# Kernel optimization log

Hardware: AMD Instinct MI355X
Metric: run time of the kernel (lower is better)

## Reference

```python
import jax, jax.numpy as jnp
from jax import lax
import numpy as np

B, T, Z, H, W = 4, 256, 16, 64, 64

def setup_inputs() -> dict:
    key = jax.random.key(0)
    k1, k2, k3, k4, k5 = jax.random.split(key, 5)
    # per-pixel scalar RNN parameters (nn.RNN(1, 1) per pixel)
    return {
        "x": jax.random.normal(k1, (B, T, Z, H, W), dtype=jnp.float32),
        "w_ih": jax.random.normal(k2, (Z, H, W), dtype=jnp.float32),
        "w_hh": jax.random.normal(k3, (Z, H, W), dtype=jnp.float32),
        "b_ih": jax.random.normal(k4, (Z, H, W), dtype=jnp.float32),
        "b_hh": jax.random.normal(k5, (Z, H, W), dtype=jnp.float32),
    }

def reference(x, w_ih, w_hh, b_ih, b_hh):
    # x: (B, T, Z, H, W). Per-pixel scalar tanh-RNN, h0 = 0:
    #   h_t = tanh(w_ih * x_t + b_ih + w_hh * h_{t-1} + b_hh)
    xt = jnp.moveaxis(x, 1, 0)  # (T, B, Z, H, W) for scan over time
    bias = b_ih + b_hh          # fuse biases once

    def step(h, x_t):
        h_new = jnp.tanh(x_t * w_ih + h * w_hh + bias)
        return h_new, h_new

    h0 = jnp.zeros(xt.shape[1:], dtype=x.dtype)  # (B, Z, H, W)
    _, ys = lax.scan(step, h0, xt)               # ys: (T, B, Z, H, W)
    return jnp.moveaxis(ys, 0, 1)                # (B, T, Z, H, W)
```

## Files before the change

kernel.cpp:

```cpp
#include <hip/hip_runtime.h>


#define RNN_B   4
#define RNN_T   256
#define RNN_ZHW 65536
#define RNN_PG4 (RNN_ZHW / 4)
#define PF_D    8

typedef float f32x4 __attribute__((ext_vector_type(4)));

__device__ __forceinline__ float fast_tanh(float x) {
    float e = __builtin_amdgcn_exp2f(x * 2.885390081777927f);
    float r = __builtin_amdgcn_rcpf(e + 1.0f);
    return fmaf(-2.0f, r, 1.0f);
}

__global__ __launch_bounds__(256) void pixel_rnn_kernel(
    const float* __restrict__ x,
    const float* __restrict__ w_ih,
    const float* __restrict__ w_hh,
    const float* __restrict__ b_ih,
    const float* __restrict__ b_hh,
    float* __restrict__ out)
{
    const int g  = blockIdx.x * 256 + threadIdx.x;
    const int b  = g >> 14;
    const int pg = g & (RNN_PG4 - 1);
    const int p  = pg << 2;

    const f32x4 wi = *(const f32x4*)(w_ih + p);
    const f32x4 wh = *(const f32x4*)(w_hh + p);
    const f32x4 bi = *(const f32x4*)(b_ih + p);
    const f32x4 bh = *(const f32x4*)(b_hh + p);
    const f32x4 bias = bi + bh;

    const f32x4* __restrict__ xp = (const f32x4*)x + (size_t)b * (RNN_T * RNN_PG4) + pg;
    f32x4* __restrict__ op       = (f32x4*)out     + (size_t)b * (RNN_T * RNN_PG4) + pg;

    f32x4 h = {0.f, 0.f, 0.f, 0.f};

    f32x4 buf[PF_D];
#pragma unroll
    for (int j = 0; j < PF_D; ++j)
        buf[j] = __builtin_nontemporal_load(xp + (size_t)j * RNN_PG4);

    for (int t = 0; t < RNN_T; t += PF_D) {
#pragma unroll
        for (int j = 0; j < PF_D; ++j) {
            const f32x4 xc = buf[j];
            int tn = t + j + PF_D;
            tn = tn < RNN_T ? tn : RNN_T - 1;
            buf[j] = __builtin_nontemporal_load(xp + (size_t)tn * RNN_PG4);

#pragma unroll
            for (int c = 0; c < 4; ++c)
                h[c] = fast_tanh(fmaf(wi[c], xc[c], fmaf(wh[c], h[c], bias[c])));

            __builtin_nontemporal_store(h, op + (size_t)(t + j) * RNN_PG4);
        }
    }
}

extern "C" void kernel_launch(void* const* d_in, const int* in_sizes, int n_in,
                              void* d_out, int out_size, void* d_ws, size_t ws_size,
                              hipStream_t stream) {
    const float* x    = (const float*)d_in[0];
    const float* w_ih = (const float*)d_in[1];
    const float* w_hh = (const float*)d_in[2];
    const float* b_ih = (const float*)d_in[3];
    const float* b_hh = (const float*)d_in[4];
    float* out        = (float*)d_out;

    pixel_rnn_kernel<<<dim3(RNN_B * RNN_PG4 / 256), dim3(256), 0, stream>>>(
        x, w_ih, w_hh, b_ih, b_hh, out);
}
```

Measured before the change: 434.3 us.

## Switch from float4-per-thread to scalar-per-thread pixels and peel prefetch tail

Each thread now handles one pixel instead of four, which launches four times as many threads (1024 blocks instead of 256) to raise occupancy and memory-level parallelism across the 256 CUs. Loads and stores become scalar 4-byte accesses, which stay coalesced across the wavefront but issue more memory instructions. The clamped prefetch index is replaced by a peeled final iteration, which removes the redundant tail loads.

```diff
diff --git a/kernel.cpp b/kernel.cpp
--- a/kernel.cpp
+++ b/kernel.cpp
@@ -4,10 +4,7 @@
 #define RNN_B   4
 #define RNN_T   256
 #define RNN_ZHW 65536
-#define RNN_PG4 (RNN_ZHW / 4)
 #define PF_D    8
-
-typedef float f32x4 __attribute__((ext_vector_type(4)));
 
 __device__ __forceinline__ float fast_tanh(float x) {
     float e = __builtin_amdgcn_exp2f(x * 2.885390081777927f);
@@ -23,41 +20,39 @@
     const float* __restrict__ b_hh,
     float* __restrict__ out)
 {
-    const int g  = blockIdx.x * 256 + threadIdx.x;
-    const int b  = g >> 14;
-    const int pg = g & (RNN_PG4 - 1);
-    const int p  = pg << 2;
+    const int g = blockIdx.x * 256 + threadIdx.x;
+    const int b = g >> 16;
+    const int p = g & (RNN_ZHW - 1);
 
-    const f32x4 wi = *(const f32x4*)(w_ih + p);
-    const f32x4 wh = *(const f32x4*)(w_hh + p);
-    const f32x4 bi = *(const f32x4*)(b_ih + p);
-    const f32x4 bh = *(const f32x4*)(b_hh + p);
-    const f32x4 bias = bi + bh;
+    const float wi   = w_ih[p];
+    const float wh   = w_hh[p];
+    const float bias = b_ih[p] + b_hh[p];
 
-    const f32x4* __restrict__ xp = (const f32x4*)x + (size_t)b * (RNN_T * RNN_PG4) + pg;
-    f32x4* __restrict__ op       = (f32x4*)out     + (size_t)b * (RNN_T * RNN_PG4) + pg;
+    const float* __restrict__ xp = x   + (size_t)b * (RNN_T * RNN_ZHW) + p;
+    float* __restrict__ op       = out + (size_t)b * (RNN_T * RNN_ZHW) + p;
 
-    f32x4 h = {0.f, 0.f, 0.f, 0.f};
+    float h = 0.f;
 
-    f32x4 buf[PF_D];
+    float buf[PF_D];
 #pragma unroll
     for (int j = 0; j < PF_D; ++j)
-        buf[j] = __builtin_nontemporal_load(xp + (size_t)j * RNN_PG4);
+        buf[j] = __builtin_nontemporal_load(xp + (size_t)j * RNN_ZHW);
 
-    for (int t = 0; t < RNN_T; t += PF_D) {
+    for (int t = 0; t < RNN_T - PF_D; t += PF_D) {
 #pragma unroll
         for (int j = 0; j < PF_D; ++j) {
-            const f32x4 xc = buf[j];
-            int tn = t + j + PF_D;
-            tn = tn < RNN_T ? tn : RNN_T - 1;
-            buf[j] = __builtin_nontemporal_load(xp + (size_t)tn * RNN_PG4);
+            const float xc = buf[j];
+            buf[j] = __builtin_nontemporal_load(xp + (size_t)(t + j + PF_D) * RNN_ZHW);
+
+            h = fast_tanh(fmaf(wi, xc, fmaf(wh, h, bias)));
+            __builtin_nontemporal_store(h, op + (size_t)(t + j) * RNN_ZHW);
+        }
+    }
 
 #pragma unroll
-            for (int c = 0; c < 4; ++c)
-                h[c] = fast_tanh(fmaf(wi[c], xc[c], fmaf(wh[c], h[c], bias[c])));
-
-            __builtin_nontemporal_store(h, op + (size_t)(t + j) * RNN_PG4);
-        }
+    for (int j = 0; j < PF_D; ++j) {
+        h = fast_tanh(fmaf(wi, buf[j], fmaf(wh, h, bias)));
+        __builtin_nontemporal_store(h, op + (size_t)(RNN_T - PF_D + j) * RNN_ZHW);
     }
 }
 
@@ -71,6 +66,6 @@
     const float* b_hh = (const float*)d_in[4];
     float* out        = (float*)d_out;
 
-    pixel_rnn_kernel<<<dim3(RNN_B * RNN_PG4 / 256), dim3(256), 0, stream>>>(
+    pixel_rnn_kernel<<<dim3(RNN_B * RNN_ZHW / 256), dim3(256), 0, stream>>>(
         x, w_ih, w_hh, b_ih, b_hh, out);
 }
```

After: 426.9 us. Within noise of the previous version (-1.7%).
